# Optimization experiments

Hardware: AMD Instinct MI355X
Metric: run time of the kernel (lower is better)

The kernel has to match this reference:

```python
import jax, jax.numpy as jnp
import numpy as np

L = 3000          # nodes per modality
M = 3             # modalities
N = L * M         # total nodes
E = 200000        # edges
D = 512           # hidden_dim
S = D // 4        # shared_dim = 128
EPS = 1e-12       # F.normalize eps


def _lrelu(x):
    return jax.nn.leaky_relu(x, negative_slope=0.01)


def _l2norm(x):
    n = jnp.linalg.norm(x, axis=-1, keepdims=True)
    return x / jnp.maximum(n, EPS)


def setup_inputs() -> dict:
    key = jax.random.key(0)
    ks = jax.random.split(key, 16)
    w = lambda k, shape: (jax.random.normal(k, shape, dtype=jnp.float32) * 0.02)
    inp = {
        "feat0": jax.random.normal(ks[0], (L, D), dtype=jnp.float32),
        "feat1": jax.random.normal(ks[1], (L, D), dtype=jnp.float32),
        "feat2": jax.random.normal(ks[2], (L, D), dtype=jnp.float32),
        "edge_index": jax.random.randint(ks[3], (2, E), 0, N, dtype=jnp.int64),
        # EdgeWeightGen params (torch Linear convention: weight is (out, in))
        "proj_w": w(ks[4], (S, D)),
        "mlp_w1": w(ks[5], (S, 2 * S)),
        "mlp_b1": jnp.zeros((S,), dtype=jnp.float32),
        "mlp_w2": w(ks[6], (1, S)),
        "mlp_b2": jnp.zeros((1,), dtype=jnp.float32),
        # CrossModalGraphLayer params, 2 layers
        "W1_0": w(ks[7], (D, D)),
        "W2_0": w(ks[8], (D, 2 * D)),
        "W1_1": w(ks[9], (D, D)),
        "W2_1": w(ks[10], (D, 2 * D)),
    }
    return inp


def reference(feat0, feat1, feat2, edge_index, proj_w, mlp_w1, mlp_b1,
              mlp_w2, mlp_b2, W1_0, W2_0, W1_1, W2_1):
    feature = jnp.concatenate([feat0, feat1, feat2], axis=0)  # (N, D)
    src, tgt = edge_index[0], edge_index[1]

    # EdgeWeightGen
    shared_src = _l2norm(feature[src] @ proj_w.T)   # (E, S)
    shared_tgt = _l2norm(feature[tgt] @ proj_w.T)   # (E, S)
    emb_cat = jnp.concatenate([shared_src, shared_tgt], axis=-1)  # (E, 2S)
    h = _lrelu(emb_cat @ mlp_w1.T + mlp_b1)
    edge_weight = jax.nn.sigmoid((h @ mlp_w2.T + mlp_b2)[:, 0])   # (E,)

    # build_adj_matrix: dense scatter-add (sparse_coo coalesce sums dups)
    adj = jnp.zeros((N, N), dtype=feature.dtype).at[src, tgt].add(edge_weight)
    row_sum = adj.sum(axis=1)
    d_inv_sqrt = jnp.where(row_sum > 0, row_sum ** -0.5, 0.0)
    # D^{-1/2} A D^{-1/2} as elementwise row/col scaling (same math as diag matmuls)
    gcn = d_inv_sqrt[:, None] * adj * d_inv_sqrt[None, :]

    # graph layers
    x = feature
    for W1, W2 in ((W1_0, W2_0), (W1_1, W2_1)):
        proj = x @ W1.T                 # (N, D)
        nb = gcn @ proj                 # (N, D)
        cat = jnp.concatenate([x + nb, x * nb], axis=-1)  # (N, 2D)
        x = _lrelu(cat @ W2.T)
    return x  # concatenated updated features; chunk(x, 3) recovers per-modal tuple
```

## Files before the change

kernel.cpp:

```cpp
#include <hip/hip_runtime.h>
#include <hip/hip_bf16.h>
#include <math.h>

#define NL 3000
#define NN 9000
#define NE 200000
#define DD 512
#define SS 128
#define MPAD 9088
#define MT   (MPAD/16)

typedef __attribute__((ext_vector_type(8))) short    bf16x8;
typedef __attribute__((ext_vector_type(8))) ushort   u16x8;
typedef __attribute__((ext_vector_type(4))) float    f32x4;

static __device__ __forceinline__ ushort f2bf(float f){
  unsigned u = __float_as_uint(f);
  return (ushort)((u + 0x7FFFu + ((u>>16)&1u)) >> 16);
}
static __device__ __forceinline__ float bf2f(ushort u){
  return __uint_as_float(((unsigned)u)<<16);
}

__global__ __launch_bounds__(256) void k_cpack(const float* __restrict__ f0, const float* __restrict__ f1,
                                               const float* __restrict__ f2,
                                               float* __restrict__ feat, short* __restrict__ P){
  int t = blockIdx.x*4 + (threadIdx.x>>6);
  int lane = threadIdx.x & 63;
  int tm = t >> 4, tk = t & 15;
  int m = tm*16 + (lane&15);
  int k = tk*32 + (lane>>4)*8;
  float4 v0 = make_float4(0,0,0,0), v1 = v0;
  if (m < NN){
    const float* srow = (m < NL) ? f0 + (size_t)m*DD
                       : (m < 2*NL) ? f1 + (size_t)(m-NL)*DD
                       : f2 + (size_t)(m-2*NL)*DD;
    v0 = *(const float4*)(srow + k);
    v1 = *(const float4*)(srow + k + 4);
    *(float4*)(feat + (size_t)m*DD + k)     = v0;
    *(float4*)(feat + (size_t)m*DD + k + 4) = v1;
  }
  u16x8 r;
  r[0]=f2bf(v0.x); r[1]=f2bf(v0.y); r[2]=f2bf(v0.z); r[3]=f2bf(v0.w);
  r[4]=f2bf(v1.x); r[5]=f2bf(v1.y); r[6]=f2bf(v1.z); r[7]=f2bf(v1.w);
  *(u16x8*)(P + (size_t)t*512 + lane*8) = r;
}

__global__ __launch_bounds__(256) void k_pack(const float* __restrict__ X, short* __restrict__ P,
                                              int M, int K, int nTilesK){
  int t = blockIdx.x*4 + (threadIdx.x>>6);
  int lane = threadIdx.x & 63;
  int tm = t / nTilesK, tk = t - tm*nTilesK;
  int m = tm*16 + (lane&15);
  int k = tk*32 + (lane>>4)*8;
  float4 v0 = make_float4(0,0,0,0), v1 = v0;
  if (m < M){
    v0 = *(const float4*)(X + (size_t)m*K + k);
    v1 = *(const float4*)(X + (size_t)m*K + k + 4);
  }
  u16x8 r;
  r[0]=f2bf(v0.x); r[1]=f2bf(v0.y); r[2]=f2bf(v0.z); r[3]=f2bf(v0.w);
  r[4]=f2bf(v1.x); r[5]=f2bf(v1.y); r[6]=f2bf(v1.z); r[7]=f2bf(v1.w);
  *(u16x8*)(P + (size_t)t*512 + lane*8) = r;
}

__global__ __launch_bounds__(256) void k_wpack5(const float* __restrict__ pw,
                                                const float* __restrict__ W10, const float* __restrict__ W20,
                                                const float* __restrict__ W11, const float* __restrict__ W21,
                                                short* __restrict__ BpF,
                                                short* __restrict__ Bp10, short* __restrict__ Bp20,
                                                short* __restrict__ Bp11, short* __restrict__ Bp21){
  int t = blockIdx.x*4 + (threadIdx.x>>6);
  int lane = threadIdx.x & 63;
  const float* X; short* P; int K, ntk, lt;
  if (t < 128)      { X=pw;  P=BpF;  K=512;  ntk=16; lt=t; }
  else if (t < 640) { X=W10; P=Bp10; K=512;  ntk=16; lt=t-128; }
  else if (t < 1664){ X=W20; P=Bp20; K=1024; ntk=32; lt=t-640; }
  else if (t < 2176){ X=W11; P=Bp11; K=512;  ntk=16; lt=t-1664; }
  else              { X=W21; P=Bp21; K=1024; ntk=32; lt=t-2176; }
  int tm = lt/ntk, tk = lt - tm*ntk;
  int m = tm*16 + (lane&15);
  int k = tk*32 + (lane>>4)*8;
  float4 v0 = *(const float4*)(X + (size_t)m*K + k);
  float4 v1 = *(const float4*)(X + (size_t)m*K + k + 4);
  u16x8 r;
  r[0]=f2bf(v0.x); r[1]=f2bf(v0.y); r[2]=f2bf(v0.z); r[3]=f2bf(v0.w);
  r[4]=f2bf(v1.x); r[5]=f2bf(v1.y); r[6]=f2bf(v1.z); r[7]=f2bf(v1.w);
  *(u16x8*)(P + (size_t)lt*512 + lane*8) = r;
}

__global__ __launch_bounds__(256) void k_pack_w1(const float* __restrict__ w1, short* __restrict__ P){
  int t = blockIdx.x*4 + (threadIdx.x>>6);
  int lane = threadIdx.x & 63;
  int tn = t >> 2, tk = t & 3;
  int n = tn*16 + (lane&15);
  int k = tk*32 + (lane>>4)*8;
  const float* sp = (n<128) ? (w1 + (size_t)n*256 + k) : (w1 + (size_t)(n-128)*256 + 128 + k);
  float4 v0 = *(const float4*)sp;
  float4 v1 = *(const float4*)(sp+4);
  u16x8 r;
  r[0]=f2bf(v0.x); r[1]=f2bf(v0.y); r[2]=f2bf(v0.z); r[3]=f2bf(v0.w);
  r[4]=f2bf(v1.x); r[5]=f2bf(v1.y); r[6]=f2bf(v1.z); r[7]=f2bf(v1.w);
  *(u16x8*)(P + (size_t)t*512 + lane*8) = r;
}

__global__ __launch_bounds__(256) void k_cat_pack(const float* __restrict__ x, const float* __restrict__ nb,
                                                  short* __restrict__ P){
  const int nTilesK = 32;
  int t = blockIdx.x*4 + (threadIdx.x>>6);
  int lane = threadIdx.x & 63;
  int tm = t / nTilesK, tk = t - tm*nTilesK;
  int m = tm*16 + (lane&15);
  int k = tk*32 + (lane>>4)*8;
  int kk = k & 511;
  bool mul = (k >= 512);
  float4 x0 = make_float4(0,0,0,0), x1 = x0, n0 = x0, n1 = x0;
  if (m < NN){
    x0 = *(const float4*)(x + (size_t)m*DD + kk);
    x1 = *(const float4*)(x + (size_t)m*DD + kk + 4);
    n0 = *(const float4*)(nb + (size_t)m*DD + kk);
    n1 = *(const float4*)(nb + (size_t)m*DD + kk + 4);
  }
  float v[8];
  if (mul){
    v[0]=x0.x*n0.x; v[1]=x0.y*n0.y; v[2]=x0.z*n0.z; v[3]=x0.w*n0.w;
    v[4]=x1.x*n1.x; v[5]=x1.y*n1.y; v[6]=x1.z*n1.z; v[7]=x1.w*n1.w;
  } else {
    v[0]=x0.x+n0.x; v[1]=x0.y+n0.y; v[2]=x0.z+n0.z; v[3]=x0.w+n0.w;
    v[4]=x1.x+n1.x; v[5]=x1.y+n1.y; v[6]=x1.z+n1.z; v[7]=x1.w+n1.w;
  }
  u16x8 r;
  #pragma unroll
  for (int j=0;j<8;++j) r[j]=f2bf(v[j]);
  *(u16x8*)(P + (size_t)t*512 + lane*8) = r;
}

template<int ACT, int OBF>
__global__ __launch_bounds__(256) void k_gmm(const short* __restrict__ Ap, const short* __restrict__ Bp,
                                             void* __restrict__ Cv, int M, int N, int K){
  int lane = threadIdx.x & 63, wave = threadIdx.x >> 6;
  int ktiles = K >> 5;
  int bm = blockIdx.y*128 + wave*32;
  int bn = blockIdx.x*64;
  const bf16x8* a0 = (const bf16x8*)(Ap + ((size_t)((bm>>4)  ) * ktiles)*512 + lane*8);
  const bf16x8* a1 = (const bf16x8*)(Ap + ((size_t)((bm>>4)+1) * ktiles)*512 + lane*8);
  const bf16x8* b0 = (const bf16x8*)(Bp + ((size_t)((bn>>4)  ) * ktiles)*512 + lane*8);
  const bf16x8* b1 = (const bf16x8*)(Bp + ((size_t)((bn>>4)+1) * ktiles)*512 + lane*8);
  const bf16x8* b2 = (const bf16x8*)(Bp + ((size_t)((bn>>4)+2) * ktiles)*512 + lane*8);
  const bf16x8* b3 = (const bf16x8*)(Bp + ((size_t)((bn>>4)+3) * ktiles)*512 + lane*8);
  f32x4 acc[2][4];
  #pragma unroll
  for (int i=0;i<2;++i)
    #pragma unroll
    for (int j=0;j<4;++j) acc[i][j] = (f32x4){0.f,0.f,0.f,0.f};

  for (int kt=0; kt<ktiles; ++kt){
    int off = kt*64;
    bf16x8 A0 = a0[off], A1 = a1[off];
    bf16x8 B0 = b0[off], B1 = b1[off], B2 = b2[off], B3 = b3[off];
    acc[0][0] = __builtin_amdgcn_mfma_f32_16x16x32_bf16(A0, B0, acc[0][0], 0,0,0);
    acc[0][1] = __builtin_amdgcn_mfma_f32_16x16x32_bf16(A0, B1, acc[0][1], 0,0,0);
    acc[0][2] = __builtin_amdgcn_mfma_f32_16x16x32_bf16(A0, B2, acc[0][2], 0,0,0);
    acc[0][3] = __builtin_amdgcn_mfma_f32_16x16x32_bf16(A0, B3, acc[0][3], 0,0,0);
    acc[1][0] = __builtin_amdgcn_mfma_f32_16x16x32_bf16(A1, B0, acc[1][0], 0,0,0);
    acc[1][1] = __builtin_amdgcn_mfma_f32_16x16x32_bf16(A1, B1, acc[1][1], 0,0,0);
    acc[1][2] = __builtin_amdgcn_mfma_f32_16x16x32_bf16(A1, B2, acc[1][2], 0,0,0);
    acc[1][3] = __builtin_amdgcn_mfma_f32_16x16x32_bf16(A1, B3, acc[1][3], 0,0,0);
  }
  int colo = lane & 15;
  int rowo = (lane >> 4) * 4;
  #pragma unroll
  for (int mi=0; mi<2; ++mi){
    #pragma unroll
    for (int r=0; r<4; ++r){
      int row = bm + mi*16 + rowo + r;
      if (row < M){
        #pragma unroll
        for (int ni=0; ni<4; ++ni){
          float v = acc[mi][ni][r];
          if (ACT) v = v>0.f ? v : 0.01f*v;
          int cidx = bn + ni*16 + colo;
          if (OBF) ((ushort*)Cv)[(size_t)row*N + cidx] = f2bf(v);
          else     ((float*) Cv)[(size_t)row*N + cidx] = v;
        }
      }
    }
  }
}

__global__ __launch_bounds__(256) void k_l2n(const float* __restrict__ X, short* __restrict__ ShP){
  int lane = threadIdx.x & 63, wave = threadIdx.x >> 6;
  int m = blockIdx.x*4 + wave;
  float2 v = ((const float2*)(X + (size_t)m*SS))[lane];
  float ss = v.x*v.x + v.y*v.y;
  #pragma unroll
  for (int o=32;o>0;o>>=1) ss += __shfl_xor(ss, o);
  float inv = 1.f / fmaxf(sqrtf(ss), 1e-12f);
  int k = 2*lane;
  int tIdx = (m>>4)*4 + (k>>5);
  int pos  = ((m&15) + ((k>>3)&3)*16)*8 + (k&7);
  ushort2 r; r.x = f2bf(v.x*inv); r.y = f2bf(v.y*inv);
  *(ushort2*)(ShP + (size_t)tIdx*512 + pos) = r;
}

__global__ __launch_bounds__(256) void k_edge(const int* __restrict__ src, const int* __restrict__ tgt,
                      const ushort* __restrict__ AB,
                      const float* __restrict__ b1, const float* __restrict__ w2,
                      const float* __restrict__ b2p,
                      float* __restrict__ ew, float* __restrict__ row_sum, int* __restrict__ cnt){
  int lane = threadIdx.x & 63;
  int p = lane & 15, g = lane >> 4;
  int wid = blockIdx.x*(blockDim.x>>6) + (threadIdx.x>>6);
  int nw  = gridDim.x*(blockDim.x>>6);
  float4 b1a = ((const float4*)b1)[p*2], b1b = ((const float4*)b1)[p*2+1];
  float4 w2a = ((const float4*)w2)[p*2], w2b = ((const float4*)w2)[p*2+1];
  float bb[8] = {b1a.x,b1a.y,b1a.z,b1a.w,b1b.x,b1b.y,b1b.z,b1b.w};
  float ww[8] = {w2a.x,w2a.y,w2a.z,w2a.w,w2b.x,w2b.y,w2b.z,w2b.w};
  float b2 = b2p[0];
  for (int e = wid*4+g; e < NE; e += nw*4){
    int s = src[e], tg_ = tgt[e];
    u16x8 av = *(const u16x8*)(AB + (size_t)s*256 + p*8);
    u16x8 bv = *(const u16x8*)(AB + (size_t)tg_*256 + 128 + p*8);
    float acc = 0.f;
    #pragma unroll
    for (int i=0;i<8;++i){
      float h = bf2f(av[i]) + bf2f(bv[i]) + bb[i];
      h = h>0.f ? h : 0.01f*h;
      acc += h*ww[i];
    }
    acc += __shfl_xor(acc,1); acc += __shfl_xor(acc,2);
    acc += __shfl_xor(acc,4); acc += __shfl_xor(acc,8);
    if (p==0){
      float wgt = 1.f/(1.f+expf(-(acc+b2)));
      ew[e]=wgt;
      atomicAdd(&row_sum[s], wgt);
      atomicAdd(&cnt[s], 1);
    }
  }
}

__global__ __launch_bounds__(1024) void k_scan(const int* __restrict__ cnt, const float* __restrict__ row_sum,
                      int* __restrict__ row_ptr, float* __restrict__ dinv, int* __restrict__ fill){
  __shared__ int wsum[16];
  int t = threadIdx.x;
  int lane = t & 63, wid = t >> 6;
  const int CH = 9;
  int base = t*CH;
  int v[CH]; int s = 0;
  #pragma unroll
  for (int i=0;i<CH;++i){
    int idx = base+i;
    v[i] = (idx<NN) ? cnt[idx] : 0;
    s += v[i];
  }
  int ps = s;
  #pragma unroll
  for (int o=1;o<64;o<<=1){
    int x = __shfl_up(ps, o);
    if (lane >= o) ps += x;
  }
  if (lane==63) wsum[wid] = ps;
  __syncthreads();
  if (wid==0){
    int wv = (lane<16)? wsum[lane] : 0;
    #pragma unroll
    for (int o=1;o<16;o<<=1){
      int x = __shfl_up(wv, o);
      if (lane>=o) wv += x;
    }
    if (lane<16) wsum[lane]=wv;
  }
  __syncthreads();
  int prefix = (wid>0 ? wsum[wid-1] : 0) + (ps - s);
  #pragma unroll
  for (int i=0;i<CH;++i){
    int idx = base+i;
    if (idx<NN){
      row_ptr[idx] = prefix;
      float rs = row_sum[idx];
      dinv[idx] = rs>0.f ? (1.f/sqrtf(rs)) : 0.f;
      fill[idx] = 0;
      prefix += v[i];
    }
  }
  if (t==1023) row_ptr[NN] = wsum[15];
}

__global__ __launch_bounds__(256) void k_scatter(const int* __restrict__ src, const int* __restrict__ tgt,
                        const float* __restrict__ ew, const float* __restrict__ dinv,
                        const int* __restrict__ row_ptr, int* __restrict__ fill,
                        int* __restrict__ col, float* __restrict__ coef){
  int e = blockIdx.x*blockDim.x+threadIdx.x;
  if (e>=NE) return;
  int s=src[e], tg=tgt[e];
  int pos = atomicAdd(&fill[s],1);
  int idx = row_ptr[s]+pos;
  col[idx]=tg;
  coef[idx]=dinv[s]*ew[e]*dinv[tg];
}

__global__ __launch_bounds__(128) void k_spmm_bf(const int* __restrict__ row_ptr, const int* __restrict__ col,
                     const float* __restrict__ coef, const ushort* __restrict__ proj,
                     float* __restrict__ nb){
  int m = blockIdx.x, t = threadIdx.x;
  int beg = row_ptr[m], end = row_ptr[m+1];
  float4 a0 = make_float4(0,0,0,0), a1 = a0, a2 = a0, a3 = a0;
  int j = beg;
  for (; j+4<=end; j+=4){
    int c0=col[j], c1=col[j+1], c2=col[j+2], c3=col[j+3];
    float w0=coef[j], w1=coef[j+1], w2_=coef[j+2], w3=coef[j+3];
    ushort4 p0 = ((const ushort4*)(proj + (size_t)c0*DD))[t];
    ushort4 p1 = ((const ushort4*)(proj + (size_t)c1*DD))[t];
    ushort4 p2 = ((const ushort4*)(proj + (size_t)c2*DD))[t];
    ushort4 p3 = ((const ushort4*)(proj + (size_t)c3*DD))[t];
    a0.x += w0*bf2f(p0.x); a0.y += w0*bf2f(p0.y); a0.z += w0*bf2f(p0.z); a0.w += w0*bf2f(p0.w);
    a1.x += w1*bf2f(p1.x); a1.y += w1*bf2f(p1.y); a1.z += w1*bf2f(p1.z); a1.w += w1*bf2f(p1.w);
    a2.x += w2_*bf2f(p2.x); a2.y += w2_*bf2f(p2.y); a2.z += w2_*bf2f(p2.z); a2.w += w2_*bf2f(p2.w);
    a3.x += w3*bf2f(p3.x); a3.y += w3*bf2f(p3.y); a3.z += w3*bf2f(p3.z); a3.w += w3*bf2f(p3.w);
  }
  for (; j<end; ++j){
    int c0=col[j]; float w0=coef[j];
    ushort4 p0 = ((const ushort4*)(proj + (size_t)c0*DD))[t];
    a0.x += w0*bf2f(p0.x); a0.y += w0*bf2f(p0.y); a0.z += w0*bf2f(p0.z); a0.w += w0*bf2f(p0.w);
  }
  a0.x += a1.x + a2.x + a3.x;
  a0.y += a1.y + a2.y + a3.y;
  a0.z += a1.z + a2.z + a3.z;
  a0.w += a1.w + a2.w + a3.w;
  ((float4*)(nb + (size_t)m*DD))[t] = a0;
}

extern "C" void kernel_launch(void* const* d_in, const int* in_sizes, int n_in,
                              void* d_out, int out_size, void* d_ws, size_t ws_size,
                              hipStream_t stream){
  const float* f0 = (const float*)d_in[0];
  const float* f1 = (const float*)d_in[1];
  const float* f2 = (const float*)d_in[2];
  const int*   ei = (const int*)d_in[3];
  const float* pw = (const float*)d_in[4];
  const float* w1 = (const float*)d_in[5];
  const float* b1 = (const float*)d_in[6];
  const float* w2 = (const float*)d_in[7];
  const float* b2 = (const float*)d_in[8];
  const float* W1_0 = (const float*)d_in[9];
  const float* W2_0 = (const float*)d_in[10];
  const float* W1_1 = (const float*)d_in[11];
  const float* W2_1 = (const float*)d_in[12];
  float* out = (float*)d_out;

  const int* src = ei;
  const int* tgt = ei + NE;

  char* base = (char*)d_ws;
  size_t o = 0;
  auto alloc = [&](size_t bytes)->char*{ char* p = base + o; o += (bytes + 1023) & ~size_t(1023); return p; };
  float* feature = (float*)alloc((size_t)NN*DD*4);
  float* x1      = (float*)alloc((size_t)NN*DD*4);
  float* nb      = (float*)alloc((size_t)NN*DD*4);
  ushort* projbf = (ushort*)alloc((size_t)NN*DD*2);
  float* projS   = (float*)alloc((size_t)NN*SS*4);
  ushort* ABn    = (ushort*)alloc((size_t)NN*256*2);
  short* Apack1  = (short*)alloc((size_t)MT*16*1024);
  short* Apack2  = (short*)alloc((size_t)MT*32*1024);
  short* ShP     = (short*)alloc((size_t)MT*4*1024);
  short* BpF     = (short*)alloc((size_t)8*16*1024);
  short* Bpab    = (short*)alloc((size_t)16*4*1024);
  short* Bp10    = (short*)alloc((size_t)32*16*1024);
  short* Bp20    = (short*)alloc((size_t)32*32*1024);
  short* Bp11    = (short*)alloc((size_t)32*16*1024);
  short* Bp21    = (short*)alloc((size_t)32*32*1024);
  float* ew      = (float*)alloc(NE*4);
  float* coef    = (float*)alloc(NE*4);
  float* row_sum = (float*)alloc(NN*4);
  int*   cnt     = (int*)alloc(NN*4);
  float* dinv    = (float*)alloc(NN*4);
  int*   fill    = (int*)alloc(NN*4);
  int*   row_ptr = (int*)alloc((NN+1)*4);
  int*   col     = (int*)alloc(NE*4);

  hipMemsetAsync(row_sum, 0, NN*4, stream);
  hipMemsetAsync(cnt, 0, NN*4, stream);

  k_cpack<<<MT*16/4, 256, 0, stream>>>(f0,f1,f2,feature,Apack1);
  k_wpack5<<<800, 256, 0, stream>>>(pw,W1_0,W2_0,W1_1,W2_1,BpF,Bp10,Bp20,Bp11,Bp21);
  k_pack_w1<<<16, 256, 0, stream>>>(w1, Bpab);

  dim3 gF(128/64, MPAD/128);
  k_gmm<0,0><<<gF, 256, 0, stream>>>(Apack1, BpF, projS, NN, 128, 512);
  k_l2n<<<NN/4, 256, 0, stream>>>(projS, ShP);
  dim3 gAB(256/64, MPAD/128);
  k_gmm<0,1><<<gAB, 256, 0, stream>>>(ShP, Bpab, ABn, NN, 256, 128);

  k_edge<<<2048, 256, 0, stream>>>(src,tgt,ABn,b1,w2,b2,ew,row_sum,cnt);
  k_scan<<<1, 1024, 0, stream>>>(cnt,row_sum,row_ptr,dinv,fill);
  k_scatter<<<(NE+255)/256, 256, 0, stream>>>(src,tgt,ew,dinv,row_ptr,fill,col,coef);

  dim3 gg(512/64, MPAD/128);
  k_gmm<0,1><<<gg, 256, 0, stream>>>(Apack1, Bp10, projbf, NN, DD, DD);
  k_spmm_bf<<<NN, 128, 0, stream>>>(row_ptr, col, coef, projbf, nb);
  k_cat_pack<<<MT*32/4, 256, 0, stream>>>(feature, nb, Apack2);
  k_gmm<1,0><<<gg, 256, 0, stream>>>(Apack2, Bp20, x1, NN, DD, 2*DD);
  k_pack<<<MT*16/4, 256, 0, stream>>>(x1, Apack1, NN, DD, 16);
  k_gmm<0,1><<<gg, 256, 0, stream>>>(Apack1, Bp11, projbf, NN, DD, DD);
  k_spmm_bf<<<NN, 128, 0, stream>>>(row_ptr, col, coef, projbf, nb);
  k_cat_pack<<<MT*32/4, 256, 0, stream>>>(x1, nb, Apack2);
  k_gmm<1,0><<<gg, 256, 0, stream>>>(Apack2, Bp21, out, NN, DD, 2*DD);
}
```

Before: 359.7 us.

## Fuse SpMM with concat-pack and drop the fp32 feature copy

```diff
diff --git a/kernel.cpp b/kernel.cpp
--- a/kernel.cpp
+++ b/kernel.cpp
@@ -23,8 +23,7 @@
 }
 
 __global__ __launch_bounds__(256) void k_cpack(const float* __restrict__ f0, const float* __restrict__ f1,
-                                               const float* __restrict__ f2,
-                                               float* __restrict__ feat, short* __restrict__ P){
+                                               const float* __restrict__ f2, short* __restrict__ P){
   int t = blockIdx.x*4 + (threadIdx.x>>6);
   int lane = threadIdx.x & 63;
   int tm = t >> 4, tk = t & 15;
@@ -37,8 +36,6 @@
                        : f2 + (size_t)(m-2*NL)*DD;
     v0 = *(const float4*)(srow + k);
     v1 = *(const float4*)(srow + k + 4);
-    *(float4*)(feat + (size_t)m*DD + k)     = v0;
-    *(float4*)(feat + (size_t)m*DD + k + 4) = v1;
   }
   u16x8 r;
   r[0]=f2bf(v0.x); r[1]=f2bf(v0.y); r[2]=f2bf(v0.z); r[3]=f2bf(v0.w);
@@ -101,37 +98,6 @@
   u16x8 r;
   r[0]=f2bf(v0.x); r[1]=f2bf(v0.y); r[2]=f2bf(v0.z); r[3]=f2bf(v0.w);
   r[4]=f2bf(v1.x); r[5]=f2bf(v1.y); r[6]=f2bf(v1.z); r[7]=f2bf(v1.w);
-  *(u16x8*)(P + (size_t)t*512 + lane*8) = r;
-}
-
-__global__ __launch_bounds__(256) void k_cat_pack(const float* __restrict__ x, const float* __restrict__ nb,
-                                                  short* __restrict__ P){
-  const int nTilesK = 32;
-  int t = blockIdx.x*4 + (threadIdx.x>>6);
-  int lane = threadIdx.x & 63;
-  int tm = t / nTilesK, tk = t - tm*nTilesK;
-  int m = tm*16 + (lane&15);
-  int k = tk*32 + (lane>>4)*8;
-  int kk = k & 511;
-  bool mul = (k >= 512);
-  float4 x0 = make_float4(0,0,0,0), x1 = x0, n0 = x0, n1 = x0;
-  if (m < NN){
-    x0 = *(const float4*)(x + (size_t)m*DD + kk);
-    x1 = *(const float4*)(x + (size_t)m*DD + kk + 4);
-    n0 = *(const float4*)(nb + (size_t)m*DD + kk);
-    n1 = *(const float4*)(nb + (size_t)m*DD + kk + 4);
-  }
-  float v[8];
-  if (mul){
-    v[0]=x0.x*n0.x; v[1]=x0.y*n0.y; v[2]=x0.z*n0.z; v[3]=x0.w*n0.w;
-    v[4]=x1.x*n1.x; v[5]=x1.y*n1.y; v[6]=x1.z*n1.z; v[7]=x1.w*n1.w;
-  } else {
-    v[0]=x0.x+n0.x; v[1]=x0.y+n0.y; v[2]=x0.z+n0.z; v[3]=x0.w+n0.w;
-    v[4]=x1.x+n1.x; v[5]=x1.y+n1.y; v[6]=x1.z+n1.z; v[7]=x1.w+n1.w;
-  }
-  u16x8 r;
-  #pragma unroll
-  for (int j=0;j<8;++j) r[j]=f2bf(v[j]);
   *(u16x8*)(P + (size_t)t*512 + lane*8) = r;
 }
 
@@ -299,9 +265,12 @@
   coef[idx]=dinv[s]*ew[e]*dinv[tg];
 }
 
-__global__ __launch_bounds__(128) void k_spmm_bf(const int* __restrict__ row_ptr, const int* __restrict__ col,
+template<int LAYER>
+__global__ __launch_bounds__(128) void k_spmm_cat(const int* __restrict__ row_ptr, const int* __restrict__ col,
                      const float* __restrict__ coef, const ushort* __restrict__ proj,
-                     float* __restrict__ nb){
+                     const float* __restrict__ xf0, const float* __restrict__ xf1,
+                     const float* __restrict__ xf2,
+                     short* __restrict__ P){
   int m = blockIdx.x, t = threadIdx.x;
   int beg = row_ptr[m], end = row_ptr[m+1];
   float4 a0 = make_float4(0,0,0,0), a1 = a0, a2 = a0, a3 = a0;
@@ -327,7 +296,24 @@
   a0.y += a1.y + a2.y + a3.y;
   a0.z += a1.z + a2.z + a3.z;
   a0.w += a1.w + a2.w + a3.w;
-  ((float4*)(nb + (size_t)m*DD))[t] = a0;
+  const float* xrow;
+  if (LAYER==0){
+    xrow = (m < NL) ? xf0 + (size_t)m*DD
+         : (m < 2*NL) ? xf1 + (size_t)(m-NL)*DD
+         : xf2 + (size_t)(m-2*NL)*DD;
+  } else {
+    xrow = xf0 + (size_t)m*DD;
+  }
+  float4 xv = ((const float4*)xrow)[t];
+  float ax = xv.x + a0.x, ay = xv.y + a0.y, az = xv.z + a0.z, aw = xv.w + a0.w;
+  float mx = xv.x * a0.x, my = xv.y * a0.y, mz = xv.z * a0.z, mw = xv.w * a0.w;
+  ushort4 ra, rm;
+  ra.x=f2bf(ax); ra.y=f2bf(ay); ra.z=f2bf(az); ra.w=f2bf(aw);
+  rm.x=f2bf(mx); rm.y=f2bf(my); rm.z=f2bf(mz); rm.w=f2bf(mw);
+  size_t tileA = (size_t)((m>>4)*32 + (t>>3));
+  int    off   = ((m&15) + ((t>>1)&3)*16)*8 + (t&1)*4;
+  *(ushort4*)(P + tileA*512 + off)        = ra;
+  *(ushort4*)(P + (tileA+16)*512 + off)   = rm;
 }
 
 extern "C" void kernel_launch(void* const* d_in, const int* in_sizes, int n_in,
@@ -354,9 +340,7 @@
   char* base = (char*)d_ws;
   size_t o = 0;
   auto alloc = [&](size_t bytes)->char*{ char* p = base + o; o += (bytes + 1023) & ~size_t(1023); return p; };
-  float* feature = (float*)alloc((size_t)NN*DD*4);
   float* x1      = (float*)alloc((size_t)NN*DD*4);
-  float* nb      = (float*)alloc((size_t)NN*DD*4);
   ushort* projbf = (ushort*)alloc((size_t)NN*DD*2);
   float* projS   = (float*)alloc((size_t)NN*SS*4);
   ushort* ABn    = (ushort*)alloc((size_t)NN*256*2);
@@ -381,7 +365,7 @@
   hipMemsetAsync(row_sum, 0, NN*4, stream);
   hipMemsetAsync(cnt, 0, NN*4, stream);
 
-  k_cpack<<<MT*16/4, 256, 0, stream>>>(f0,f1,f2,feature,Apack1);
+  k_cpack<<<MT*16/4, 256, 0, stream>>>(f0,f1,f2,Apack1);
   k_wpack5<<<800, 256, 0, stream>>>(pw,W1_0,W2_0,W1_1,W2_1,BpF,Bp10,Bp20,Bp11,Bp21);
   k_pack_w1<<<16, 256, 0, stream>>>(w1, Bpab);
 
@@ -397,12 +381,10 @@
 
   dim3 gg(512/64, MPAD/128);
   k_gmm<0,1><<<gg, 256, 0, stream>>>(Apack1, Bp10, projbf, NN, DD, DD);
-  k_spmm_bf<<<NN, 128, 0, stream>>>(row_ptr, col, coef, projbf, nb);
-  k_cat_pack<<<MT*32/4, 256, 0, stream>>>(feature, nb, Apack2);
+  k_spmm_cat<0><<<NN, 128, 0, stream>>>(row_ptr, col, coef, projbf, f0, f1, f2, Apack2);
   k_gmm<1,0><<<gg, 256, 0, stream>>>(Apack2, Bp20, x1, NN, DD, 2*DD);
   k_pack<<<MT*16/4, 256, 0, stream>>>(x1, Apack1, NN, DD, 16);
   k_gmm<0,1><<<gg, 256, 0, stream>>>(Apack1, Bp11, projbf, NN, DD, DD);
-  k_spmm_bf<<<NN, 128, 0, stream>>>(row_ptr, col, coef, projbf, nb);
-  k_cat_pack<<<MT*32/4, 256, 0, stream>>>(x1, nb, Apack2);
+  k_spmm_cat<1><<<NN, 128, 0, stream>>>(row_ptr, col, coef, projbf, x1, nullptr, nullptr, Apack2);
   k_gmm<1,0><<<gg, 256, 0, stream>>>(Apack2, Bp21, out, NN, DD, 2*DD);
 }
```

New measurement: 353.8 us. Within noise of the previous version (-1.6%).
